# Kernel tuning notes

Hardware: AMD Instinct MI355X
Metric: run time of the kernel (lower is better)

The kernel has to match this reference:

```python
import jax, jax.numpy as jnp
import numpy as np

B, S, D, H, FF = 2, 4096, 512, 8, 2048
HD = D // H
EPS = 1e-5


def setup_inputs() -> dict:
    key = jax.random.key(0)
    ks = jax.random.split(key, 14)
    init = lambda k, shape: jax.random.normal(k, shape, dtype=jnp.float32) * 0.02
    return {
        "x": jax.random.normal(ks[0], (B, S, D), dtype=jnp.float32),
        "Wq": init(ks[1], (D, D)), "bq": jnp.zeros((D,), jnp.float32),
        "Wk": init(ks[2], (D, D)), "bk": jnp.zeros((D,), jnp.float32),
        "Wv": init(ks[3], (D, D)), "bv": jnp.zeros((D,), jnp.float32),
        "Wo": init(ks[4], (D, D)), "bo": jnp.zeros((D,), jnp.float32),
        "W1": init(ks[5], (D, FF)), "b1": jnp.zeros((FF,), jnp.float32),
        "W2": init(ks[6], (FF, D)), "b2": jnp.zeros((D,), jnp.float32),
        "g1": jnp.ones((D,), jnp.float32), "beta1": jnp.zeros((D,), jnp.float32),
        "g2": jnp.ones((D,), jnp.float32), "beta2": jnp.zeros((D,), jnp.float32),
    }


def layer_norm(x, g, b):
    mu = jnp.mean(x, axis=-1, keepdims=True)
    var = jnp.mean(jnp.square(x - mu), axis=-1, keepdims=True)
    return (x - mu) * jax.lax.rsqrt(var + EPS) * g + b


def reference(x, Wq, bq, Wk, bk, Wv, bv, Wo, bo, W1, b1, W2, b2, g1, beta1, g2, beta2):
    # --- pre-LN self-attention block ---
    residual = x
    h = layer_norm(x, g1, beta1)
    # project and split heads: [B, H, S, HD]
    q = (h @ Wq + bq).reshape(B, S, H, HD).transpose(0, 2, 1, 3)
    k = (h @ Wk + bk).reshape(B, S, H, HD).transpose(0, 2, 1, 3)
    v = (h @ Wv + bv).reshape(B, S, H, HD).transpose(0, 2, 1, 3)
    scale = HD ** -0.5
    scores = jnp.einsum('bhqd,bhkd->bhqk', q, k) * scale  # [B,H,S,S] materialized
    attn = jax.nn.softmax(scores, axis=-1)
    ctx = jnp.einsum('bhqk,bhkd->bhqd', attn, v)
    ctx = ctx.transpose(0, 2, 1, 3).reshape(B, S, D)
    attn_out = ctx @ Wo + bo
    x = residual + attn_out  # dropout p=0.0 -> identity
    # --- pre-LN FFN block ---
    residual = x
    h = layer_norm(x, g2, beta2)
    h = jax.nn.gelu(h @ W1 + b1, approximate=False)  # nn.GELU default = exact erf
    h = h @ W2 + b2
    x = residual + h
    return (x, attn)
```

## Files before the change

### kernel.cpp

```cpp
#include <hip/hip_runtime.h>
#include <hip/hip_bf16.h>

#define B_ 2
#define S_ 4096
#define D_ 512
#define H_ 8
#define HD_ 64
#define FF_ 2048
#define NT_ (B_*S_)
#define EPS_ 1e-5f

typedef __attribute__((ext_vector_type(8))) short bf16x8;
typedef __attribute__((ext_vector_type(4))) float f32x4;
typedef __attribute__((ext_vector_type(4))) unsigned int u32x4;

__device__ __forceinline__ short f2bf(float f){
  __hip_bfloat16 h = __float2bfloat16(f);
  return __builtin_bit_cast(short, h);
}
__device__ __forceinline__ float bf2f(short s){
  return __bfloat162float(__builtin_bit_cast(__hip_bfloat16, s));
}
__device__ __forceinline__ unsigned pack2(float lo, float hi){
  return ((unsigned)(unsigned short)f2bf(hi) << 16) | (unsigned short)f2bf(lo);
}
__device__ __forceinline__ void load8(const float* p, float* f){
  f32x4 a = *(const f32x4*)p; f32x4 b = *(const f32x4*)(p+4);
  #pragma unroll
  for (int j=0;j<4;j++){ f[j]=a[j]; f[4+j]=b[j]; }
}
__device__ __forceinline__ void load8(const short* p, float* f){
  bf16x8 v = *(const bf16x8*)p;
  #pragma unroll
  for (int j=0;j<8;j++) f[j]=bf2f(v[j]);
}
__device__ __forceinline__ float ldval(const float* p, size_t i){ return p[i]; }
__device__ __forceinline__ float ldval(const short* p, size_t i){ return bf2f(p[i]); }
__device__ __forceinline__ void stval(float* p, size_t i, float v){ p[i]=v; }
__device__ __forceinline__ void stval(short* p, size_t i, float v){ p[i]=f2bf(v); }

#define GLL(src, dst) __builtin_amdgcn_global_load_lds( \
    (const __attribute__((address_space(1))) void*)(src), \
    (__attribute__((address_space(3))) void*)(dst), 16, 0, 0)

__global__ __launch_bounds__(256) void transpose_bf(const float* __restrict__ W,
                                                    short* __restrict__ WT, int K, int N){
  __shared__ float tile[32][33];
  int n0 = blockIdx.x*32, k0 = blockIdx.y*32;
  int tx = threadIdx.x, ty = threadIdx.y;
  #pragma unroll
  for (int i=0;i<32;i+=8)
    tile[ty+i][tx] = W[(size_t)(k0+ty+i)*N + n0+tx];
  __syncthreads();
  #pragma unroll
  for (int i=0;i<32;i+=8)
    WT[(size_t)(n0+ty+i)*K + k0+tx] = f2bf(tile[tx][ty+i]);
}

__global__ __launch_bounds__(256) void transpose_v(const short* __restrict__ V,
                                                   short* __restrict__ VT){
  __shared__ short tile[32][33];
  int d0 = blockIdx.x*32, s0 = blockIdx.y*32, bh = blockIdx.z;
  int b = bh >> 3, h = bh & (H_-1);
  const short* Vp = V + (size_t)b*S_*D_ + (size_t)h*HD_;
  short* VTp = VT + (size_t)bh*HD_*S_;
  int tx = threadIdx.x, ty = threadIdx.y;
  #pragma unroll
  for (int i=0;i<32;i+=8)
    tile[ty+i][tx] = Vp[(size_t)(s0+ty+i)*D_ + d0+tx];
  __syncthreads();
  #pragma unroll
  for (int i=0;i<32;i+=8)
    VTp[(size_t)(d0+ty+i)*S_ + s0+tx] = tile[tx][ty+i];
}

template<typename TIn>
__global__ __launch_bounds__(256) void ln_kernel(const TIn* __restrict__ X,
                                                 const float* __restrict__ G,
                                                 const float* __restrict__ Bt,
                                                 short* __restrict__ O){
  int wid = threadIdx.x>>6, lane = threadIdx.x&63;
  int tok = blockIdx.x*4 + wid;
  const TIn* xp = X + (size_t)tok*D_;
  float f[8]; load8(xp + lane*8, f);
  float s=0.f, s2=0.f;
  #pragma unroll
  for (int j=0;j<8;j++){ s+=f[j]; s2+=f[j]*f[j]; }
  #pragma unroll
  for (int m=1;m<64;m<<=1){ s += __shfl_xor(s,m); s2 += __shfl_xor(s2,m); }
  float mu = s*(1.f/D_);
  float var = s2*(1.f/D_) - mu*mu;
  float rr = rsqrtf(var + EPS_);
  f32x4 g0 = *(const f32x4*)(G + lane*8), g1v = *(const f32x4*)(G + lane*8 + 4);
  f32x4 b0 = *(const f32x4*)(Bt + lane*8), b1v = *(const f32x4*)(Bt + lane*8 + 4);
  bf16x8 o;
  #pragma unroll
  for (int j=0;j<4;j++){
    o[j]   = f2bf((f[j]-mu)*rr*g0[j]  + b0[j]);
    o[4+j] = f2bf((f[4+j]-mu)*rr*g1v[j] + b1v[j]);
  }
  *(bf16x8*)(O + (size_t)tok*D_ + lane*8) = o;
}

template<int EPI, typename TR, typename TO>
__global__ __launch_bounds__(256) void gemm_bt(const short* __restrict__ A,
                                               const short* __restrict__ BT,
                                               const float* __restrict__ bias,
                                               const TR* __restrict__ res,
                                               TO* __restrict__ out,
                                               int M, int N, int K){
  __shared__ short As[128][40];
  __shared__ short Bs[128][40];
  int m0 = blockIdx.y*128, n0 = blockIdx.x*128;
  int tid = threadIdx.x, lane = tid&63, wid = tid>>6;
  int wr = wid>>1, wc = wid&1;
  int r = lane&15, kk = (lane>>4)*8;
  int arow = tid>>2, acol = (tid&3)*8;
  f32x4 zero = {0.f,0.f,0.f,0.f};
  f32x4 acc[4][4];
  #pragma unroll
  for (int i=0;i<4;i++)
    #pragma unroll
    for (int j=0;j<4;j++) acc[i][j] = zero;

  for (int k0=0;k0<K;k0+=32){
    __syncthreads();
    *(bf16x8*)&As[arow][acol]    = *(const bf16x8*)&A [(size_t)(m0+arow)*K    + k0+acol];
    *(bf16x8*)&As[arow+64][acol] = *(const bf16x8*)&A [(size_t)(m0+arow+64)*K + k0+acol];
    *(bf16x8*)&Bs[arow][acol]    = *(const bf16x8*)&BT[(size_t)(n0+arow)*K    + k0+acol];
    *(bf16x8*)&Bs[arow+64][acol] = *(const bf16x8*)&BT[(size_t)(n0+arow+64)*K + k0+acol];
    __syncthreads();
    bf16x8 a[4], b[4];
    #pragma unroll
    for (int i=0;i<4;i++) a[i] = *(const bf16x8*)&As[wr*64+i*16+r][kk];
    #pragma unroll
    for (int i=0;i<4;i++) b[i] = *(const bf16x8*)&Bs[wc*64+i*16+r][kk];
    #pragma unroll
    for (int mi=0;mi<4;mi++)
      #pragma unroll
      for (int ni=0;ni<4;ni++)
        acc[mi][ni] = __builtin_amdgcn_mfma_f32_16x16x32_bf16(a[mi], b[ni], acc[mi][ni], 0,0,0);
  }
  #pragma unroll
  for (int mi=0;mi<4;mi++){
    #pragma unroll
    for (int ni=0;ni<4;ni++){
      int col = n0 + wc*64 + ni*16 + r;
      float bs = bias[col];
      #pragma unroll
      for (int j=0;j<4;j++){
        int row = m0 + wr*64 + mi*16 + (lane>>4)*4 + j;
        float v = acc[mi][ni][j] + bs;
        if (EPI==1) v += ldval(res, (size_t)row*N + col);
        if (EPI==2) v = 0.5f*v*(1.f + erff(v*0.70710678118f));
        stval(out, (size_t)row*N + col, v);
      }
    }
  }
}

template<int EPI, typename TR, typename TO>
__global__ __launch_bounds__(256) void gemm_bt64(const short* __restrict__ A,
                                                 const short* __restrict__ BT,
                                                 const float* __restrict__ bias,
                                                 const TR* __restrict__ res,
                                                 TO* __restrict__ out,
                                                 int M, int N, int K){
  __shared__ short As[128][40];
  __shared__ short Bs[64][40];
  int m0 = blockIdx.y*128, n0 = blockIdx.x*64;
  int tid = threadIdx.x, lane = tid&63, wid = tid>>6;
  int wr = wid>>1, wc = wid&1;
  int r = lane&15, kk = (lane>>4)*8;
  int arow = tid>>2, acol = (tid&3)*8;
  f32x4 zero = {0.f,0.f,0.f,0.f};
  f32x4 acc[4][2];
  #pragma unroll
  for (int i=0;i<4;i++){ acc[i][0] = zero; acc[i][1] = zero; }

  for (int k0=0;k0<K;k0+=32){
    __syncthreads();
    *(bf16x8*)&As[arow][acol]    = *(const bf16x8*)&A [(size_t)(m0+arow)*K    + k0+acol];
    *(bf16x8*)&As[arow+64][acol] = *(const bf16x8*)&A [(size_t)(m0+arow+64)*K + k0+acol];
    *(bf16x8*)&Bs[arow][acol]    = *(const bf16x8*)&BT[(size_t)(n0+arow)*K    + k0+acol];
    __syncthreads();
    bf16x8 a[4], b[2];
    #pragma unroll
    for (int i=0;i<4;i++) a[i] = *(const bf16x8*)&As[wr*64+i*16+r][kk];
    #pragma unroll
    for (int j=0;j<2;j++) b[j] = *(const bf16x8*)&Bs[wc*32+j*16+r][kk];
    #pragma unroll
    for (int mi=0;mi<4;mi++)
      #pragma unroll
      for (int nj=0;nj<2;nj++)
        acc[mi][nj] = __builtin_amdgcn_mfma_f32_16x16x32_bf16(a[mi], b[nj], acc[mi][nj], 0,0,0);
  }
  #pragma unroll
  for (int mi=0;mi<4;mi++){
    #pragma unroll
    for (int nj=0;nj<2;nj++){
      int col = n0 + wc*32 + nj*16 + r;
      float bs = bias[col];
      #pragma unroll
      for (int j=0;j<4;j++){
        int row = m0 + wr*64 + mi*16 + (lane>>4)*4 + j;
        float v = acc[mi][nj][j] + bs;
        if (EPI==1) v += ldval(res, (size_t)row*N + col);
        if (EPI==2) v = 0.5f*v*(1.f + erff(v*0.70710678118f));
        stval(out, (size_t)row*N + col, v);
      }
    }
  }
}

__global__ __launch_bounds__(256, 2) void attn_kernel(const short* __restrict__ Q,
                                                      const short* __restrict__ Kt,
                                                      const short* __restrict__ VT,
                                                      float* __restrict__ attn_o,
                                                      short* __restrict__ ctx){
  __shared__ __align__(16) char smem[65536];
  __shared__ float dcomb[4][4][16];
  int wid = threadIdx.x>>6, lane = threadIdx.x&63;
  int bh = blockIdx.y, b = bh>>3, h = bh&7;
  int q0 = blockIdx.x*64;
  int r = lane&15, qh = lane>>4;
  bool hi4 = (lane>>4)&1, hi5 = (lane>>5)&1;
  const short* Qp = Q  + (size_t)b*S_*D_ + (size_t)h*HD_;
  const short* Kp = Kt + (size_t)b*S_*D_ + (size_t)h*HD_;
  const short* Vp = VT + (size_t)bh*HD_*S_;
  float* Ap = attn_o + (size_t)bh*S_*S_;

  char* stg = smem + wid*16384;
  short* KB0 = (short*)stg;         short* KB1 = (short*)(stg+4096);
  short* VB0 = (short*)(stg+8192);  short* VB1 = (short*)(stg+12288);

  #define SCOF(n) (wid*32 + (n)*128)

  auto stageK = [&](int sc, short* buf){
    #pragma unroll
    for (int i=0;i<4;i++){
      int row = i*8 + (lane>>3);
      int col = ((lane&7)*8) ^ ((row&7)*8);
      GLL(&Kp[(size_t)(sc+row)*D_ + col], buf + i*512);
    }
  };
  auto stageV = [&](int sc, short* buf){
    #pragma unroll
    for (int i=0;i<4;i++){
      int d = i*16 + (lane>>2);
      int col = ((lane&3)*8) ^ ((d&3)*8);
      GLL(&Vp[(size_t)d*S_ + sc + col], buf + i*512);
    }
  };
  const int kc0 = (qh*16) ^ ((r&7)<<4);
  const int kc1 = (64 + qh*16) ^ ((r&7)<<4);
  const int vc  = (qh*16) ^ ((r&3)<<4);

  bf16x8 aq[4][2];
  #pragma unroll
  for (int qt=0;qt<4;qt++){
    aq[qt][0] = *(const bf16x8*)&Qp[(size_t)(q0+qt*16+r)*D_ + qh*8];
    aq[qt][1] = *(const bf16x8*)&Qp[(size_t)(q0+qt*16+r)*D_ + 32 + qh*8];
  }
  const f32x4 zero = {0.f,0.f,0.f,0.f};

  float part[4] = {0.f,0.f,0.f,0.f};

#define S1BODY(n, NW, DOSTG) { \
  asm volatile("s_waitcnt vmcnt(" #NW ")" ::: "memory"); \
  short* kb_ = ((n)&1)? KB1 : KB0; \
  bf16x8 kf0 = *(const bf16x8*)((char*)kb_ + r*128 + kc0); \
  bf16x8 kf1 = *(const bf16x8*)((char*)kb_ + r*128 + kc1); \
  bf16x8 kf2 = *(const bf16x8*)((char*)kb_ + (16+r)*128 + kc0); \
  bf16x8 kf3 = *(const bf16x8*)((char*)kb_ + (16+r)*128 + kc1); \
  asm volatile("s_waitcnt lgkmcnt(0)" ::: "memory"); \
  if (DOSTG) stageK(SCOF((n)+2), kb_); \
  _Pragma("unroll") \
  for (int qt=0;qt<4;qt++){ \
    f32x4 s0 = __builtin_amdgcn_mfma_f32_16x16x32_bf16(kf0, aq[qt][0], zero, 0,0,0); \
    s0 = __builtin_amdgcn_mfma_f32_16x16x32_bf16(kf1, aq[qt][1], s0, 0,0,0); \
    f32x4 s1 = __builtin_amdgcn_mfma_f32_16x16x32_bf16(kf2, aq[qt][0], zero, 0,0,0); \
    s1 = __builtin_amdgcn_mfma_f32_16x16x32_bf16(kf3, aq[qt][1], s1, 0,0,0); \
    _Pragma("unroll") \
    for (int j=0;j<4;j++) part[qt] += __expf(s0[j]*0.125f) + __expf(s1[j]*0.125f); \
  } \
}

  stageK(SCOF(0), KB0); stageK(SCOF(1), KB1);
  S1BODY(0,4,1)
  for (int k2=0;k2<14;k2++){ S1BODY(2*k2+1,4,1) S1BODY(2*k2+2,4,1) }
  S1BODY(29,4,1) S1BODY(30,4,0) S1BODY(31,0,0)
#undef S1BODY

  #pragma unroll
  for (int qt=0;qt<4;qt++){
    part[qt] += __shfl_xor(part[qt],16);
    part[qt] += __shfl_xor(part[qt],32);
  }
  if (lane < 16){
    #pragma unroll
    for (int qt=0;qt<4;qt++) dcomb[wid][qt][r] = part[qt];
  }
  __syncthreads();
  float invl[4];
  #pragma unroll
  for (int qt=0;qt<4;qt++)
    invl[qt] = 1.f/(dcomb[0][qt][r]+dcomb[1][qt][r]+dcomb[2][qt][r]+dcomb[3][qt][r]);

  f32x4 cacc[4][4];
  #pragma unroll
  for (int qt=0;qt<4;qt++)
    #pragma unroll
    for (int n2=0;n2<4;n2++) cacc[qt][n2] = zero;

#define S2BODY(n, NW, DOSTG) { \
  asm volatile("s_waitcnt vmcnt(" #NW ")" ::: "memory"); \
  short* kb_ = ((n)&1)? KB1 : KB0; \
  short* vb_ = ((n)&1)? VB1 : VB0; \
  int sc_ = SCOF(n); \
  bf16x8 kf0 = *(const bf16x8*)((char*)kb_ + r*128 + kc0); \
  bf16x8 kf1 = *(const bf16x8*)((char*)kb_ + r*128 + kc1); \
  bf16x8 kf2 = *(const bf16x8*)((char*)kb_ + (16+r)*128 + kc0); \
  bf16x8 kf3 = *(const bf16x8*)((char*)kb_ + (16+r)*128 + kc1); \
  bf16x8 vf0 = *(const bf16x8*)((char*)vb_ + (r)*64    + vc); \
  bf16x8 vf1 = *(const bf16x8*)((char*)vb_ + (16+r)*64 + vc); \
  bf16x8 vf2 = *(const bf16x8*)((char*)vb_ + (32+r)*64 + vc); \
  bf16x8 vf3 = *(const bf16x8*)((char*)vb_ + (48+r)*64 + vc); \
  asm volatile("s_waitcnt lgkmcnt(0)" ::: "memory"); \
  if (DOSTG){ stageK(SCOF((n)+2), kb_); stageV(SCOF((n)+2), vb_); } \
  _Pragma("unroll") \
  for (int qt=0;qt<4;qt++){ \
    f32x4 s0 = __builtin_amdgcn_mfma_f32_16x16x32_bf16(kf0, aq[qt][0], zero, 0,0,0); \
    s0 = __builtin_amdgcn_mfma_f32_16x16x32_bf16(kf1, aq[qt][1], s0, 0,0,0); \
    f32x4 s1 = __builtin_amdgcn_mfma_f32_16x16x32_bf16(kf2, aq[qt][0], zero, 0,0,0); \
    s1 = __builtin_amdgcn_mfma_f32_16x16x32_bf16(kf3, aq[qt][1], s1, 0,0,0); \
    float e0[4], e1[4]; \
    _Pragma("unroll") \
    for (int j=0;j<4;j++){ \
      e0[j] = __expf(s0[j]*0.125f)*invl[qt]; \
      e1[j] = __expf(s1[j]*0.125f)*invl[qt]; \
    } \
    f32x4 o0 = {e0[0],e0[1],e0[2],e0[3]}; \
    f32x4 o1 = {e1[0],e1[1],e1[2],e1[3]}; \
    float* dst = &Ap[(size_t)(q0+qt*16+r)*S_ + sc_ + qh*4]; \
    *(f32x4*)dst = o0; \
    *(f32x4*)(dst+16) = o1; \
    unsigned v0 = pack2(e0[0],e0[1]), v1 = pack2(e0[2],e0[3]); \
    unsigned v2 = pack2(e1[0],e1[1]), v3 = pack2(e1[2],e1[3]); \
    unsigned u0 = __shfl_xor((int)v0,16), u1 = __shfl_xor((int)v1,16); \
    unsigned u2 = __shfl_xor((int)v2,16), u3 = __shfl_xor((int)v3,16); \
    unsigned s0c0 = hi4?u0:v0, s0c1 = hi4?u1:v1, s0c2 = hi4?v0:u0, s0c3 = hi4?v1:u1; \
    unsigned s1c0 = hi4?u2:v2, s1c1 = hi4?u3:v3, s1c2 = hi4?v2:u2, s1c3 = hi4?v3:u3; \
    unsigned w0 = hi5?s0c0:s1c0, w1 = hi5?s0c1:s1c1, w2 = hi5?s0c2:s1c2, w3 = hi5?s0c3:s1c3; \
    unsigned wp0 = __shfl_xor((int)w0,32), wp1 = __shfl_xor((int)w1,32); \
    unsigned wp2 = __shfl_xor((int)w2,32), wp3 = __shfl_xor((int)w3,32); \
    u32x4 pw; \
    pw[0] = (qh==0)?s0c0:(qh==3)?s1c0:wp0; \
    pw[1] = (qh==0)?s0c1:(qh==3)?s1c1:wp1; \
    pw[2] = (qh==0)?s0c2:(qh==3)?s1c2:wp2; \
    pw[3] = (qh==0)?s0c3:(qh==3)?s1c3:wp3; \
    bf16x8 pa = __builtin_bit_cast(bf16x8, pw); \
    cacc[qt][0] = __builtin_amdgcn_mfma_f32_16x16x32_bf16(pa, vf0, cacc[qt][0], 0,0,0); \
    cacc[qt][1] = __builtin_amdgcn_mfma_f32_16x16x32_bf16(pa, vf1, cacc[qt][1], 0,0,0); \
    cacc[qt][2] = __builtin_amdgcn_mfma_f32_16x16x32_bf16(pa, vf2, cacc[qt][2], 0,0,0); \
    cacc[qt][3] = __builtin_amdgcn_mfma_f32_16x16x32_bf16(pa, vf3, cacc[qt][3], 0,0,0); \
  } \
}

  stageK(SCOF(0), KB0); stageV(SCOF(0), VB0);
  stageK(SCOF(1), KB1); stageV(SCOF(1), VB1);
  S2BODY(0,8,1)
  for (int k2=0;k2<14;k2++){ S2BODY(2*k2+1,16,1) S2BODY(2*k2+2,16,1) }
  S2BODY(29,16,1) S2BODY(30,16,0) S2BODY(31,8,0)
#undef S2BODY
#undef SCOF

  __syncthreads();
  float* cmb = (float*)smem;
  if (wid & 1){
    float* dstp = cmb + (wid>>1)*4096;
    #pragma unroll
    for (int qt=0;qt<4;qt++)
      #pragma unroll
      for (int n2=0;n2<4;n2++)
        #pragma unroll
        for (int j=0;j<4;j++)
          dstp[(qt*16+qh*4+j)*64 + n2*16 + r] = cacc[qt][n2][j];
  }
  __syncthreads();
  if (!(wid & 1)){
    float* srcp = cmb + (wid>>1)*4096;
    #pragma unroll
    for (int qt=0;qt<4;qt++)
      #pragma unroll
      for (int n2=0;n2<4;n2++)
        #pragma unroll
        for (int j=0;j<4;j++)
          cacc[qt][n2][j] += srcp[(qt*16+qh*4+j)*64 + n2*16 + r];
  }
  __syncthreads();
  if (wid == 2){
    #pragma unroll
    for (int qt=0;qt<4;qt++)
      #pragma unroll
      for (int n2=0;n2<4;n2++)
        #pragma unroll
        for (int j=0;j<4;j++)
          cmb[(qt*16+qh*4+j)*64 + n2*16 + r] = cacc[qt][n2][j];
  }
  __syncthreads();
  if (wid == 0){
    #pragma unroll
    for (int qt=0;qt<4;qt++)
      #pragma unroll
      for (int n2=0;n2<4;n2++)
        #pragma unroll
        for (int j=0;j<4;j++){
          float v = cacc[qt][n2][j] + cmb[(qt*16+qh*4+j)*64 + n2*16 + r];
          ctx[(size_t)(b*S_ + q0 + qt*16 + qh*4 + j)*D_ + h*HD_ + n2*16 + r] = f2bf(v);
        }
  }
}

extern "C" void kernel_launch(void* const* d_in, const int* in_sizes, int n_in,
                              void* d_out, int out_size, void* d_ws, size_t ws_size,
                              hipStream_t stream){
  const float* x   = (const float*)d_in[0];
  const float* Wq  = (const float*)d_in[1];
  const float* bq  = (const float*)d_in[2];
  const float* Wk  = (const float*)d_in[3];
  const float* bk  = (const float*)d_in[4];
  const float* Wv  = (const float*)d_in[5];
  const float* bv  = (const float*)d_in[6];
  const float* Wo  = (const float*)d_in[7];
  const float* bo  = (const float*)d_in[8];
  const float* W1  = (const float*)d_in[9];
  const float* b1  = (const float*)d_in[10];
  const float* W2  = (const float*)d_in[11];
  const float* b2  = (const float*)d_in[12];
  const float* g1  = (const float*)d_in[13];
  const float* be1 = (const float*)d_in[14];
  const float* g2  = (const float*)d_in[15];
  const float* be2 = (const float*)d_in[16];

  char* ws = (char*)d_ws;
  const size_t KB = 1024;
  short* wqT = (short*)(ws + 0*KB);
  short* wkT = (short*)(ws + 512*KB);
  short* wvT = (short*)(ws + 1024*KB);
  short* woT = (short*)(ws + 1536*KB);
  short* w1T = (short*)(ws + 2048*KB);
  short* w2T = (short*)(ws + 4096*KB);
  short* hbf = (short*)(ws + 6144*KB);
  short* Qb  = (short*)(ws + 14336*KB);
  short* Kb  = (short*)(ws + 22528*KB);
  short* Vb  = (short*)(ws + 30720*KB);
  short* VTb = (short*)(ws + 38912*KB);
  short* ctx = (short*)(ws + 47104*KB);
  short* f1  = (short*)(ws + 14336*KB);

  float* out0 = (float*)d_out;
  float* attn = out0 + (size_t)NT_*D_;

  dim3 tb(32,8);
  transpose_bf<<<dim3(16,16),tb,0,stream>>>(Wq, wqT, 512, 512);
  transpose_bf<<<dim3(16,16),tb,0,stream>>>(Wk, wkT, 512, 512);
  transpose_bf<<<dim3(16,16),tb,0,stream>>>(Wv, wvT, 512, 512);
  transpose_bf<<<dim3(16,16),tb,0,stream>>>(Wo, woT, 512, 512);
  transpose_bf<<<dim3(64,16),tb,0,stream>>>(W1, w1T, 512, 2048);
  transpose_bf<<<dim3(16,64),tb,0,stream>>>(W2, w2T, 2048, 512);

  ln_kernel<float><<<NT_/4, 256, 0, stream>>>(x, g1, be1, hbf);

  gemm_bt64<0,float,short><<<dim3(8,64),256,0,stream>>>(hbf, wqT, bq, nullptr, Qb, NT_, 512, 512);
  gemm_bt64<0,float,short><<<dim3(8,64),256,0,stream>>>(hbf, wkT, bk, nullptr, Kb, NT_, 512, 512);
  gemm_bt64<0,float,short><<<dim3(8,64),256,0,stream>>>(hbf, wvT, bv, nullptr, Vb, NT_, 512, 512);

  transpose_v<<<dim3(2,128,16),tb,0,stream>>>(Vb, VTb);

  attn_kernel<<<dim3(64,16), 256, 0, stream>>>(Qb, Kb, VTb, attn, ctx);

  gemm_bt64<1,float,float><<<dim3(8,64),256,0,stream>>>(ctx, woT, bo, x, out0, NT_, 512, 512);

  ln_kernel<float><<<NT_/4, 256, 0, stream>>>(out0, g2, be2, hbf);

  gemm_bt<2,float,short><<<dim3(16,64),256,0,stream>>>(hbf, w1T, b1, nullptr, f1, NT_, 2048, 512);

  gemm_bt64<1,float,float><<<dim3(8,64),256,0,stream>>>(f1, w2T, b2, out0, out0, NT_, 512, 2048);
}
```

Before: 554.7 us.

## Single-buffer V staging in attention kernel to fit three blocks per CU

```diff
diff --git a/kernel.cpp b/kernel.cpp
--- a/kernel.cpp
+++ b/kernel.cpp
@@ -213,12 +213,12 @@
   }
 }
 
-__global__ __launch_bounds__(256, 2) void attn_kernel(const short* __restrict__ Q,
+__global__ __launch_bounds__(256, 3) void attn_kernel(const short* __restrict__ Q,
                                                       const short* __restrict__ Kt,
                                                       const short* __restrict__ VT,
                                                       float* __restrict__ attn_o,
                                                       short* __restrict__ ctx){
-  __shared__ __align__(16) char smem[65536];
+  __shared__ __align__(16) char smem[49152];
   __shared__ float dcomb[4][4][16];
   int wid = threadIdx.x>>6, lane = threadIdx.x&63;
   int bh = blockIdx.y, b = bh>>3, h = bh&7;
@@ -230,9 +230,9 @@
   const short* Vp = VT + (size_t)bh*HD_*S_;
   float* Ap = attn_o + (size_t)bh*S_*S_;
 
-  char* stg = smem + wid*16384;
-  short* KB0 = (short*)stg;         short* KB1 = (short*)(stg+4096);
-  short* VB0 = (short*)(stg+8192);  short* VB1 = (short*)(stg+12288);
+  char* stg = smem + wid*12288;
+  short* KA = (short*)stg;          short* KB = (short*)(stg+4096);
+  short* VB = (short*)(stg+8192);
 
   #define SCOF(n) (wid*32 + (n)*128)
 
@@ -244,12 +244,12 @@
       GLL(&Kp[(size_t)(sc+row)*D_ + col], buf + i*512);
     }
   };
-  auto stageV = [&](int sc, short* buf){
+  auto stageV = [&](int sc){
     #pragma unroll
     for (int i=0;i<4;i++){
       int d = i*16 + (lane>>2);
       int col = ((lane&3)*8) ^ ((d&3)*8);
-      GLL(&Vp[(size_t)d*S_ + sc + col], buf + i*512);
+      GLL(&Vp[(size_t)d*S_ + sc + col], VB + i*512);
     }
   };
   const int kc0 = (qh*16) ^ ((r&7)<<4);
@@ -268,7 +268,7 @@
 
 #define S1BODY(n, NW, DOSTG) { \
   asm volatile("s_waitcnt vmcnt(" #NW ")" ::: "memory"); \
-  short* kb_ = ((n)&1)? KB1 : KB0; \
+  short* kb_ = ((n)&1)? KB : KA; \
   bf16x8 kf0 = *(const bf16x8*)((char*)kb_ + r*128 + kc0); \
   bf16x8 kf1 = *(const bf16x8*)((char*)kb_ + r*128 + kc1); \
   bf16x8 kf2 = *(const bf16x8*)((char*)kb_ + (16+r)*128 + kc0); \
@@ -286,7 +286,7 @@
   } \
 }
 
-  stageK(SCOF(0), KB0); stageK(SCOF(1), KB1);
+  stageK(SCOF(0), KA); stageK(SCOF(1), KB);
   S1BODY(0,4,1)
   for (int k2=0;k2<14;k2++){ S1BODY(2*k2+1,4,1) S1BODY(2*k2+2,4,1) }
   S1BODY(29,4,1) S1BODY(30,4,0) S1BODY(31,0,0)
@@ -313,21 +313,21 @@
     #pragma unroll
     for (int n2=0;n2<4;n2++) cacc[qt][n2] = zero;
 
-#define S2BODY(n, NW, DOSTG) { \
+#define S2BODY(n, NW, SK, SV) { \
   asm volatile("s_waitcnt vmcnt(" #NW ")" ::: "memory"); \
-  short* kb_ = ((n)&1)? KB1 : KB0; \
-  short* vb_ = ((n)&1)? VB1 : VB0; \
+  short* kb_ = ((n)&1)? KB : KA; \
   int sc_ = SCOF(n); \
   bf16x8 kf0 = *(const bf16x8*)((char*)kb_ + r*128 + kc0); \
   bf16x8 kf1 = *(const bf16x8*)((char*)kb_ + r*128 + kc1); \
   bf16x8 kf2 = *(const bf16x8*)((char*)kb_ + (16+r)*128 + kc0); \
   bf16x8 kf3 = *(const bf16x8*)((char*)kb_ + (16+r)*128 + kc1); \
-  bf16x8 vf0 = *(const bf16x8*)((char*)vb_ + (r)*64    + vc); \
-  bf16x8 vf1 = *(const bf16x8*)((char*)vb_ + (16+r)*64 + vc); \
-  bf16x8 vf2 = *(const bf16x8*)((char*)vb_ + (32+r)*64 + vc); \
-  bf16x8 vf3 = *(const bf16x8*)((char*)vb_ + (48+r)*64 + vc); \
+  bf16x8 vf0 = *(const bf16x8*)((char*)VB + (r)*64    + vc); \
+  bf16x8 vf1 = *(const bf16x8*)((char*)VB + (16+r)*64 + vc); \
+  bf16x8 vf2 = *(const bf16x8*)((char*)VB + (32+r)*64 + vc); \
+  bf16x8 vf3 = *(const bf16x8*)((char*)VB + (48+r)*64 + vc); \
   asm volatile("s_waitcnt lgkmcnt(0)" ::: "memory"); \
-  if (DOSTG){ stageK(SCOF((n)+2), kb_); stageV(SCOF((n)+2), vb_); } \
+  if (SV) stageV(SCOF((n)+1)); \
+  if (SK) stageK(SCOF((n)+2), kb_); \
   _Pragma("unroll") \
   for (int qt=0;qt<4;qt++){ \
     f32x4 s0 = __builtin_amdgcn_mfma_f32_16x16x32_bf16(kf0, aq[qt][0], zero, 0,0,0); \
@@ -367,11 +367,14 @@
   } \
 }
 
-  stageK(SCOF(0), KB0); stageV(SCOF(0), VB0);
-  stageK(SCOF(1), KB1); stageV(SCOF(1), VB1);
-  S2BODY(0,8,1)
-  for (int k2=0;k2<14;k2++){ S2BODY(2*k2+1,16,1) S2BODY(2*k2+2,16,1) }
-  S2BODY(29,16,1) S2BODY(30,16,0) S2BODY(31,8,0)
+  stageV(SCOF(0));
+  stageK(SCOF(0), KA);
+  stageK(SCOF(1), KB);
+  S2BODY(0,4,1,1)
+  for (int k2=0;k2<14;k2++){ S2BODY(2*k2+1,12,1,1) S2BODY(2*k2+2,12,1,1) }
+  S2BODY(29,12,1,1)
+  S2BODY(30,12,0,1)
+  S2BODY(31,8,0,0)
 #undef S2BODY
 #undef SCOF
 
```

Measured after the change: 689.6 us. +24.3%, slower.
